# Optimization experiments

Measured on AMD Instinct MI355X. Metric: run time of the kernel, lower is better.

## Reference

```python
import jax, jax.numpy as jnp
import numpy as np

# Kernel codes matching style 'L;O2;P2;Y2,1,1;R0.5;W1,1'
KERNEL_CODES = ['L', 'O', 'P', 'Y', 'R', 'W']
SM_TEMP = 1.0


def _norm_sq(q, k):
    # q: [n,l,h,e], k: [n,s,h,e] -> [n,h,l,s]
    q2 = jnp.einsum('nlhe,nlhe->nhl', q, q)[..., None]        # [n,h,l,1]
    k2 = jnp.einsum('nshe,nshe->nhs', k, k)[:, :, None, :]     # [n,h,1,s]
    qk = jnp.einsum('nlhe,nshe->nhls', q, k)
    return q2 + k2 - 2.0 * qk


def _kernel(code, q, k):
    if code == 'L':
        return jnp.einsum('nlhe,nshe->nhls', q, k)
    if code == 'O':  # -log(1 + ns^(p/2)), p=2
        return -jnp.log1p(_norm_sq(q, k))
    if code == 'P':  # -(ns)^(p/2), p=2
        return -_norm_sq(q, k)
    if code == 'Y':  # (alpha*<q,k> + c)^p, p=2, alpha=1, c=1
        d = jnp.einsum('nlhe,nshe->nhls', q, k)
        return (d + 1.0) ** 2
    if code == 'R':  # exp(-gamma*ns), gamma=0.5
        return jnp.exp(-0.5 * _norm_sq(q, k))
    if code == 'W':  # cos(ns/a)*exp(-ns/b), a=b=1
        ns = _norm_sq(q, k)
        return jnp.cos(ns) * jnp.exp(-ns)
    raise ValueError(code)


def setup_inputs() -> dict:
    key = jax.random.key(0)
    k1, k2, k3, k4 = jax.random.split(key, 4)
    N, L, S, H, E, K = 2, 1024, 1024, 8, 64, 6
    return {
        'query': jax.random.normal(k1, (N, L, H, E), dtype=jnp.float32),
        'key': jax.random.normal(k2, (N, S, H, E), dtype=jnp.float32),
        'attn_mask_add': jnp.zeros((N, L, S), dtype=jnp.float32),
        'key_lengths_add': jnp.zeros((N, S), dtype=jnp.float32),
        'M': jax.random.uniform(k3, (H, E, K), dtype=jnp.float32),
        'C': jax.random.uniform(k4, (K, H, E, E), dtype=jnp.float32),
    }


def reference(query, key, attn_mask_add, key_lengths_add, M, C):
    # mixture weights pi: [n,l,h,k]
    pi = jax.nn.softmax(jnp.einsum('nlhe,hek->nlhk', query, M), axis=-1)
    out = None
    for c, code in enumerate(KERNEL_CODES):
        # htilde = tanh(query @ C[c]): [n,l,h,e]
        htilde = jnp.tanh(jnp.einsum('nlhe,hef->nlhf', query, C[c]))
        qk = _kernel(code, htilde, key)                    # [n,h,l,s]
        qk = qk + attn_mask_add[:, None] + key_lengths_add[:, None, None, :]
        sm = jax.nn.softmax(SM_TEMP * qk, axis=-1)
        w = jnp.transpose(pi[..., c], (0, 2, 1))[..., None]  # [n,h,l,1]
        term = sm * w
        out = term if out is None else out + term
    return out
```

## Files before the change

kernel.cpp:

```cpp
#include <hip/hip_runtime.h>
#include <hip/hip_bf16.h>
#include <math.h>

#define N_  2
#define H_  8
#define G_  16
#define L_  1024
#define S_  1024
#define E_  64
#define NC_ 6

typedef __attribute__((ext_vector_type(4))) float floatx4;
typedef __attribute__((ext_vector_type(8))) short short8;

#define MFMA16 __builtin_amdgcn_mfma_f32_16x16x32_bf16

#define AHAT_OFF   0
#define AHAT_BYTES (NC_*G_*L_*128*2)
#define KHAT_OFF   (AHAT_OFF + AHAT_BYTES)
#define KHAT_BYTES (G_*S_*128*2)
#define PI_OFF     (KHAT_OFF + KHAT_BYTES)
#define PI_BYTES   (NC_*G_*L_*4)
#define HSQ_OFF    (PI_OFF + PI_BYTES)
#define HSQ_BYTES  (NC_*G_*L_*4)
#define KSQ_OFF    (HSQ_OFF + HSQ_BYTES)
#define KSQ_BYTES  (G_*S_*4)

__device__ __forceinline__ float ftanh(float x) {
  return 1.0f - 2.0f * __builtin_amdgcn_rcpf(__expf(2.0f*x) + 1.0f);
}

__global__ __launch_bounds__(256, 2) void k_prep(
    const float* __restrict__ q, const float* __restrict__ C,
    const float* __restrict__ key, const float* __restrict__ M,
    __hip_bfloat16* __restrict__ Ahat, float* __restrict__ hsq,
    __hip_bfloat16* __restrict__ Khat, float* __restrict__ ksq,
    float* __restrict__ pi_t) {
  extern __shared__ char smraw[];
  const int bx = blockIdx.x;
  const int t = threadIdx.x;

  if (bx < 768) {
    float* qs = (float*)smraw;
    float* Cs = qs + 128*68;
    const int g = bx / 48, r6 = bx % 48, c = r6 >> 3, lch = r6 & 7;
    const int n = g >> 3, h = g & 7;
    const int l0 = lch * 128;

    for (int u = t; u < 2048; u += 256) {
      int row = u >> 4, seg = u & 15;
      *(float4*)(qs + row*68 + seg*4) =
        *(const float4*)(q + (((size_t)(n*L_ + l0 + row))*H_ + h)*E_ + seg*4);
    }
    for (int u = t; u < 1024; u += 256) {
      int e = u >> 4, seg = u & 15;
      *(float4*)(Cs + e*68 + seg*4) =
        *(const float4*)(C + (((size_t)(c*8 + h))*64 + e)*64 + seg*4);
    }
    __syncthreads();

    const int rg = t >> 3, fg = t & 7;
    float acc[4][8];
    #pragma unroll
    for (int i = 0; i < 4; i++)
      #pragma unroll
      for (int j = 0; j < 8; j++) acc[i][j] = 0.0f;

    #pragma unroll 2
    for (int e0 = 0; e0 < 64; e0 += 4) {
      float4 q4[4];
      #pragma unroll
      for (int i = 0; i < 4; i++)
        q4[i] = *(const float4*)(qs + (rg*4 + i)*68 + e0);
      #pragma unroll
      for (int ee = 0; ee < 4; ee++) {
        float4 ca = *(const float4*)(Cs + (e0+ee)*68 + fg*8);
        float4 cb = *(const float4*)(Cs + (e0+ee)*68 + fg*8 + 4);
        float c8[8] = {ca.x, ca.y, ca.z, ca.w, cb.x, cb.y, cb.z, cb.w};
        #pragma unroll
        for (int i = 0; i < 4; i++) {
          float qv = (ee == 0) ? q4[i].x : (ee == 1) ? q4[i].y
                   : (ee == 2) ? q4[i].z : q4[i].w;
          #pragma unroll
          for (int j = 0; j < 8; j++) acc[i][j] = fmaf(qv, c8[j], acc[i][j]);
        }
      }
    }

    #pragma unroll
    for (int i = 0; i < 4; i++) {
      int l = l0 + rg*4 + i;
      size_t rowb = (((size_t)(c*G_ + g))*L_ + l) * 128;
      float ss = 0.0f;
      short8 hi8, lo8;
      #pragma unroll
      for (int j = 0; j < 8; j++) {
        float hv = ftanh(acc[i][j]);
        ss += hv*hv;
        __hip_bfloat16 hi = __float2bfloat16(hv);
        __hip_bfloat16 lo = __float2bfloat16(hv - __bfloat162float(hi));
        short hs, ls;
        __builtin_memcpy(&hs, &hi, 2);
        __builtin_memcpy(&ls, &lo, 2);
        hi8[j] = hs; lo8[j] = ls;
      }
      *(short8*)((char*)Ahat + (rowb + fg*8)*2)      = hi8;
      *(short8*)((char*)Ahat + (rowb + 64 + fg*8)*2) = lo8;
      ss += __shfl_xor(ss, 1); ss += __shfl_xor(ss, 2); ss += __shfl_xor(ss, 4);
      if (fg == 0) hsq[((size_t)(c*G_ + g))*L_ + l] = ss;
    }
  } else if (bx < 1024) {
    const int kb = bx - 768;
    const int wv = t >> 6, lane = t & 63;
    #pragma unroll 2
    for (int it = 0; it < 16; it++) {
      int r = kb*64 + it*4 + wv;
      int g = r >> 10, s = r & 1023, n = g >> 3, h = g & 7;
      float v = key[(((size_t)(n*S_ + s))*H_ + h)*E_ + lane];
      __hip_bfloat16 hi = __float2bfloat16(v);
      __hip_bfloat16 lo = __float2bfloat16(v - __bfloat162float(hi));
      size_t base = ((size_t)g*S_ + s)*128;
      Khat[base + lane]      = hi;
      Khat[base + 64 + lane] = lo;
      float sq = v*v;
      #pragma unroll
      for (int off = 32; off; off >>= 1) sq += __shfl_xor(sq, off);
      if (lane == 0) ksq[(size_t)g*S_ + s] = sq;
    }
  } else {
    float* Ms = (float*)smraw;
    const int pb = bx - 1024;
    const int g = pb >> 2, lch = pb & 3;
    const int n = g >> 3, h = g & 7;
    const int l = lch*256 + t;
    for (int u = t; u < 384; u += 256) Ms[u] = M[h*384 + u];
    __syncthreads();
    const float* qrow = q + (((size_t)(n*L_ + l))*H_ + h)*E_;
    float p[6] = {0.f, 0.f, 0.f, 0.f, 0.f, 0.f};
    #pragma unroll 8
    for (int e = 0; e < 64; e++) {
      float qv = qrow[e];
      #pragma unroll
      for (int k = 0; k < 6; k++) p[k] = fmaf(qv, Ms[e*6 + k], p[k]);
    }
    float mx = p[0];
    #pragma unroll
    for (int k = 1; k < 6; k++) mx = fmaxf(mx, p[k]);
    float den = 0.f;
    #pragma unroll
    for (int k = 0; k < 6; k++) den += __expf(p[k] - mx);
    float rden = __builtin_amdgcn_rcpf(den);
    #pragma unroll
    for (int k = 0; k < 6; k++)
      pi_t[((size_t)(k*G_ + g))*L_ + l] = __expf(p[k] - mx) * rden;
  }
}

#define LDS_A6LO  0
#define LDS_ZRED  13824
#define LDS_MRED  15360
#define LDS_CST   16896
#define LDS_TOTAL 17664

__global__ __launch_bounds__(256, 2) void k_main(
    const __hip_bfloat16* __restrict__ Ahat, const __hip_bfloat16* __restrict__ Khat,
    const float* __restrict__ hsq, const float* __restrict__ ksq,
    const float* __restrict__ mask, const float* __restrict__ klen,
    const float* __restrict__ pi_t, float* __restrict__ out) {
  extern __shared__ char smraw[];
  char*   A6     = smraw + LDS_A6LO;
  float*  zred   = (float*)(smraw + LDS_ZRED);
  float*  mred   = (float*)(smraw + LDS_MRED);
  float2* cst    = (float2*)(smraw + LDS_CST);

  const int l0 = blockIdx.x * 16; const int g = blockIdx.y; const int n = g >> 3;
  const int t = threadIdx.x; const int w = t >> 6; const int lane = t & 63;
  const int quad = lane >> 4; const int lc = lane & 15;

  #pragma unroll
  for (int rep = 0; rep < 3; rep++) {
    int u = t + rep*256; int row = u >> 3, seg = u & 7;
    int cc = row >> 4, lr = row & 15;
    *(int4*)(A6 + row*144 + seg*16) =
      *(const int4*)((const char*)Ahat +
          (((size_t)(cc*G_ + g))*L_ + l0 + lr)*256 + 128 + seg*16);
  }

  short8 ah[6][2];
  #pragma unroll
  for (int cc = 0; cc < 6; cc++) {
    const char* arow = (const char*)Ahat + (((size_t)(cc*G_ + g))*L_ + l0 + lc)*256;
    ah[cc][0] = *(const short8*)(arow + quad*16);
    ah[cc][1] = *(const short8*)(arow + 64 + quad*16);
  }

  float h1p = 1.0f  + hsq[((size_t)(1*G_ + g))*L_ + l0 + lc];
  float nh2 = 64.0f - hsq[((size_t)(2*G_ + g))*L_ + l0 + lc];
  float h4h = -0.5f * hsq[((size_t)(4*G_ + g))*L_ + l0 + lc];
  float nh5 = -hsq[((size_t)(5*G_ + g))*L_ + l0 + lc];

  __syncthreads();

  auto LOADK = [&](int st, short8 (&bf)[4]) {
    const char* base = (const char*)Khat +
        (((size_t)g)*S_ + st*64 + w*16 + lc)*256 + quad*16;
    #pragma unroll
    for (int kt = 0; kt < 4; kt++)
      bf[kt] = *(const short8*)(base + kt*64);
  };

  float Zc0 = 0.f, Zc1 = 0.f, Zc2 = 0.f, Zc3 = 0.f, zp = 0.f;
  float m3 = -INFINITY, z3 = 0.f;

  auto SWEEP1 = [&](int st, const short8 (&bf)[4]) {
    int sb = st*64 + w*16 + quad*4;
    float4 mk4 = *(const float4*)(mask + ((size_t)(n*L_ + l0 + lc))*S_ + sb);
    float4 kl4 = *(const float4*)(klen + (size_t)n*S_ + sb);
    float4 kq4 = *(const float4*)(ksq  + (size_t)g*S_ + sb);
    float kq[4] = {kq4.x, kq4.y, kq4.z, kq4.w};
    float mv[4], Ev[4];
    mv[0] = mk4.x + kl4.x; mv[1] = mk4.y + kl4.y;
    mv[2] = mk4.z + kl4.z; mv[3] = mk4.w + kl4.w;
    #pragma unroll
    for (int i = 0; i < 4; i++) Ev[i] = __expf(mv[i]);
    #pragma unroll
    for (int c = 0; c < 6; c++) {
      short8 al0 = *(const short8*)(A6 + (c*16 + lc)*144 + quad*16);
      short8 al1 = *(const short8*)(A6 + (c*16 + lc)*144 + 64 + quad*16);
      floatx4 a = {0.f, 0.f, 0.f, 0.f};
      a = MFMA16(bf[0], ah[c][0], a, 0,0,0);
      a = MFMA16(bf[1], ah[c][1], a, 0,0,0);
      a = MFMA16(bf[0], al0,      a, 0,0,0);
      a = MFMA16(bf[1], al1,      a, 0,0,0);
      a = MFMA16(bf[2], ah[c][0], a, 0,0,0);
      a = MFMA16(bf[3], ah[c][1], a, 0,0,0);
      #pragma unroll
      for (int i = 0; i < 4; i++) {
        float d = a[i];
        if (c == 0) {
          Zc0 = fmaf(Ev[i], __expf(d), Zc0);
        } else if (c == 1) {
          Zc1 = fmaf(Ev[i], __builtin_amdgcn_rcpf(fmaf(-2.f, d, h1p + kq[i])), Zc1);
        } else if (c == 2) {
          zp += __expf(fmaf(2.f, d, nh2 - kq[i] + mv[i]));
        } else if (c == 3) {
          float tt = d + 1.f;
          float x  = fmaf(tt, tt, mv[i]);
          float mn = fmaxf(m3, x);
          float e  = __expf(fminf(m3, x) - mn);
          z3 = (x > m3) ? fmaf(z3, e, 1.0f) : (z3 + e);
          m3 = mn;
        } else if (c == 4) {
          Zc2 = fmaf(Ev[i], __expf(__expf(d + fmaf(-0.5f, kq[i], h4h))), Zc2);
        } else {
          float a5 = fmaf(2.f, d, nh5 - kq[i]);
          Zc3 = fmaf(Ev[i], __expf(__cosf(a5) * __expf(a5)), Zc3);
        }
      }
    }
  };

  {
    short8 bA[4], bB[4];
    LOADK(0, bA);
    #pragma unroll 1
    for (int st = 0; st < 16; st += 2) {
      LOADK(st + 1, bB);
      SWEEP1(st, bA);
      LOADK((st + 2) & 15, bA);
      SWEEP1(st + 1, bB);
    }
  }

  #pragma unroll
  for (int off = 16; off < 64; off <<= 1) {
    Zc0 += __shfl_xor(Zc0, off); Zc1 += __shfl_xor(Zc1, off);
    Zc2 += __shfl_xor(Zc2, off); Zc3 += __shfl_xor(Zc3, off);
    zp  += __shfl_xor(zp,  off);
    float mo = __shfl_xor(m3, off);
    float zo = __shfl_xor(z3, off);
    float mn = fmaxf(m3, mo);
    float e  = __expf(fminf(m3, mo) - mn);
    z3 = (mo > m3) ? fmaf(z3, e, zo) : fmaf(zo, e, z3);
    m3 = mn;
  }
  if (lane < 16) {
    zred[w*96 + 0*16 + lc] = Zc0; mred[w*96 + 0*16 + lc] = 0.f;
    zred[w*96 + 1*16 + lc] = Zc1; mred[w*96 + 1*16 + lc] = 0.f;
    zred[w*96 + 2*16 + lc] = zp;  mred[w*96 + 2*16 + lc] = 0.f;
    zred[w*96 + 3*16 + lc] = z3;  mred[w*96 + 3*16 + lc] = m3;
    zred[w*96 + 4*16 + lc] = Zc2; mred[w*96 + 4*16 + lc] = 0.f;
    zred[w*96 + 5*16 + lc] = Zc3; mred[w*96 + 5*16 + lc] = 0.f;
  }
  __syncthreads();
  if (t < 96) {
    int c = t >> 4;
    float z = zred[t], m = mred[t];
    if (c == 3) {
      #pragma unroll
      for (int w2 = 1; w2 < 4; w2++) {
        float mo = mred[w2*96 + t], zo = zred[w2*96 + t];
        float mn = fmaxf(m, mo);
        float e  = __expf(fminf(m, mo) - mn);
        z = (mo > m) ? fmaf(z, e, zo) : fmaf(zo, e, z);
        m = mn;
      }
    } else {
      #pragma unroll
      for (int w2 = 1; w2 < 4; w2++) z += zred[w2*96 + t];
    }
    float piv = pi_t[((size_t)((t >> 4)*G_ + g))*L_ + l0 + (t & 15)];
    cst[t] = make_float2(piv / z, m);
  }
  __syncthreads();

  float ac0 = cst[0*16 + lc].x, ac1 = cst[1*16 + lc].x, ac2 = cst[2*16 + lc].x;
  float ac3 = cst[3*16 + lc].x, ac4 = cst[4*16 + lc].x, ac5 = cst[5*16 + lc].x;
  float m3f = cst[3*16 + lc].y;

  auto SWEEP2 = [&](int st, const short8 (&bf)[4]) {
    int sb = st*64 + w*16 + quad*4;
    float4 mk4 = *(const float4*)(mask + ((size_t)(n*L_ + l0 + lc))*S_ + sb);
    float4 kl4 = *(const float4*)(klen + (size_t)n*S_ + sb);
    float4 kq4 = *(const float4*)(ksq  + (size_t)g*S_ + sb);
    float kq[4] = {kq4.x, kq4.y, kq4.z, kq4.w};
    float mv[4], Ev[4];
    mv[0] = mk4.x + kl4.x; mv[1] = mk4.y + kl4.y;
    mv[2] = mk4.z + kl4.z; mv[3] = mk4.w + kl4.w;
    #pragma unroll
    for (int i = 0; i < 4; i++) Ev[i] = __expf(mv[i]);
    float Sacc[4] = {0.f, 0.f, 0.f, 0.f};
    float Gg[4]   = {0.f, 0.f, 0.f, 0.f};
    #pragma unroll
    for (int c = 0; c < 6; c++) {
      short8 al0 = *(const short8*)(A6 + (c*16 + lc)*144 + quad*16);
      short8 al1 = *(const short8*)(A6 + (c*16 + lc)*144 + 64 + quad*16);
      floatx4 a = {0.f, 0.f, 0.f, 0.f};
      a = MFMA16(bf[0], ah[c][0], a, 0,0,0);
      a = MFMA16(bf[1], ah[c][1], a, 0,0,0);
      a = MFMA16(bf[0], al0,      a, 0,0,0);
      a = MFMA16(bf[1], al1,      a, 0,0,0);
      a = MFMA16(bf[2], ah[c][0], a, 0,0,0);
      a = MFMA16(bf[3], ah[c][1], a, 0,0,0);
      #pragma unroll
      for (int i = 0; i < 4; i++) {
        float d = a[i];
        if (c == 0) {
          Sacc[i] = fmaf(ac0, __expf(d), Sacc[i]);
        } else if (c == 1) {
          Sacc[i] = fmaf(ac1, __builtin_amdgcn_rcpf(fmaf(-2.f, d, h1p + kq[i])), Sacc[i]);
        } else if (c == 2) {
          Gg[i] = fmaf(ac2, __expf(fmaf(2.f, d, nh2 - kq[i] + mv[i])), Gg[i]);
        } else if (c == 3) {
          float tt = d + 1.f;
          float x  = fmaf(tt, tt, mv[i]);
          Gg[i] = fmaf(ac3, __expf(x - m3f), Gg[i]);
        } else if (c == 4) {
          Sacc[i] = fmaf(ac4, __expf(__expf(d + fmaf(-0.5f, kq[i], h4h))), Sacc[i]);
        } else {
          float a5 = fmaf(2.f, d, nh5 - kq[i]);
          Sacc[i] = fmaf(ac5, __expf(__cosf(a5) * __expf(a5)), Sacc[i]);
        }
      }
    }
    float4 ov;
    ov.x = fmaf(Ev[0], Sacc[0], Gg[0]);
    ov.y = fmaf(Ev[1], Sacc[1], Gg[1]);
    ov.z = fmaf(Ev[2], Sacc[2], Gg[2]);
    ov.w = fmaf(Ev[3], Sacc[3], Gg[3]);
    *(float4*)(out + (((size_t)g)*L_ + l0 + lc)*S_ + sb) = ov;
  };

  {
    short8 bA[4], bB[4];
    LOADK(0, bA);
    #pragma unroll 1
    for (int st = 0; st < 16; st += 2) {
      LOADK(st + 1, bB);
      SWEEP2(st, bA);
      LOADK((st + 2) & 15, bA);
      SWEEP2(st + 1, bB);
    }
  }
}

extern "C" void kernel_launch(void* const* d_in, const int* in_sizes, int n_in,
                              void* d_out, int out_size, void* d_ws, size_t ws_size,
                              hipStream_t stream) {
  (void)in_sizes; (void)n_in; (void)out_size; (void)ws_size;
  const float* q    = (const float*)d_in[0];
  const float* key  = (const float*)d_in[1];
  const float* mask = (const float*)d_in[2];
  const float* klen = (const float*)d_in[3];
  const float* M    = (const float*)d_in[4];
  const float* C    = (const float*)d_in[5];
  char* ws = (char*)d_ws;
  __hip_bfloat16* Ahat = (__hip_bfloat16*)(ws + AHAT_OFF);
  __hip_bfloat16* Khat = (__hip_bfloat16*)(ws + KHAT_OFF);
  float* pi_t    = (float*)(ws + PI_OFF);
  float* hsq     = (float*)(ws + HSQ_OFF);
  float* ksq     = (float*)(ws + KSQ_OFF);
  float* out = (float*)d_out;

  k_prep<<<1088, 256, 52224, stream>>>(q, C, key, M, Ahat, hsq, Khat, ksq, pi_t);
  k_main<<<dim3(64, 16), 256, LDS_TOTAL, stream>>>(Ahat, Khat, hsq, ksq, mask, klen,
                                                   pi_t, out);
}
```

Baseline: 199.6 us.

## Compute htilde projection in prep kernel with split-bf16 MFMA instead of FP32 FMA

Replaces the LDS-tiled FP32 FMA matmul for query@C[c] with 16x16x32 bf16 MFMAs, using a hi/lo split (three products) to keep near-FP32 accuracy. Each wave now processes 16 rows across three of the six mixture components, reusing the query fragments it holds in registers. Dynamic shared memory for the prep kernel goes away and the grid shrinks from 1088 to 832 blocks. In exchange, C is loaded with strided, uncoalesced scalar reads and converted again for every tile, and Ahat is written with scalar 2-byte stores instead of vector stores.

Measured after the change: 207.2 us. 3.8% more time.

```diff
diff --git a/kernel.cpp b/kernel.cpp
--- a/kernel.cpp
+++ b/kernel.cpp
@@ -30,112 +30,111 @@
   return 1.0f - 2.0f * __builtin_amdgcn_rcpf(__expf(2.0f*x) + 1.0f);
 }
 
-__global__ __launch_bounds__(256, 2) void k_prep(
+__global__ __launch_bounds__(256) void k_prep(
     const float* __restrict__ q, const float* __restrict__ C,
     const float* __restrict__ key, const float* __restrict__ M,
     __hip_bfloat16* __restrict__ Ahat, float* __restrict__ hsq,
     __hip_bfloat16* __restrict__ Khat, float* __restrict__ ksq,
     float* __restrict__ pi_t) {
-  extern __shared__ char smraw[];
+  __shared__ float Ms[384];
   const int bx = blockIdx.x;
   const int t = threadIdx.x;
-
-  if (bx < 768) {
-    float* qs = (float*)smraw;
-    float* Cs = qs + 128*68;
-    const int g = bx / 48, r6 = bx % 48, c = r6 >> 3, lch = r6 & 7;
+  const int w = t >> 6, lane = t & 63;
+  const int quad = lane >> 4, lc = lane & 15;
+
+  if (bx < 512) {
+    const int g = bx >> 5, lch = bx & 31;
     const int n = g >> 3, h = g & 7;
-    const int l0 = lch * 128;
-
-    for (int u = t; u < 2048; u += 256) {
-      int row = u >> 4, seg = u & 15;
-      *(float4*)(qs + row*68 + seg*4) =
-        *(const float4*)(q + (((size_t)(n*L_ + l0 + row))*H_ + h)*E_ + seg*4);
-    }
-    for (int u = t; u < 1024; u += 256) {
-      int e = u >> 4, seg = u & 15;
-      *(float4*)(Cs + e*68 + seg*4) =
-        *(const float4*)(C + (((size_t)(c*8 + h))*64 + e)*64 + seg*4);
-    }
-    __syncthreads();
-
-    const int rg = t >> 3, fg = t & 7;
-    float acc[4][8];
-    #pragma unroll
-    for (int i = 0; i < 4; i++)
-      #pragma unroll
-      for (int j = 0; j < 8; j++) acc[i][j] = 0.0f;
-
-    #pragma unroll 2
-    for (int e0 = 0; e0 < 64; e0 += 4) {
-      float4 q4[4];
-      #pragma unroll
-      for (int i = 0; i < 4; i++)
-        q4[i] = *(const float4*)(qs + (rg*4 + i)*68 + e0);
-      #pragma unroll
-      for (int ee = 0; ee < 4; ee++) {
-        float4 ca = *(const float4*)(Cs + (e0+ee)*68 + fg*8);
-        float4 cb = *(const float4*)(Cs + (e0+ee)*68 + fg*8 + 4);
-        float c8[8] = {ca.x, ca.y, ca.z, ca.w, cb.x, cb.y, cb.z, cb.w};
+    const int lt = lch*32 + (w >> 1)*16;
+    const int c0 = (w & 1)*3;
+
+    short8 qh[2], ql[2];
+    #pragma unroll
+    for (int kc = 0; kc < 2; kc++) {
+      const float* qp = q + (((size_t)(n*L_ + lt + lc))*H_ + h)*E_ + kc*32 + quad*8;
+      float4 a0 = *(const float4*)qp, a1 = *(const float4*)(qp + 4);
+      float v[8] = {a0.x,a0.y,a0.z,a0.w,a1.x,a1.y,a1.z,a1.w};
+      #pragma unroll
+      for (int j = 0; j < 8; j++) {
+        __hip_bfloat16 hb = __float2bfloat16(v[j]);
+        __hip_bfloat16 lb = __float2bfloat16(v[j] - __bfloat162float(hb));
+        short hs, ls;
+        __builtin_memcpy(&hs, &hb, 2); __builtin_memcpy(&ls, &lb, 2);
+        qh[kc][j] = hs; ql[kc][j] = ls;
+      }
+    }
+
+    #pragma unroll 1
+    for (int cc = 0; cc < 3; cc++) {
+      const int c = c0 + cc;
+      const float* Cb = C + ((size_t)(c*8 + h))*64*64;
+      float ss[4] = {0.f, 0.f, 0.f, 0.f};
+      #pragma unroll 2
+      for (int ft = 0; ft < 4; ft++) {
+        short8 bh[2], bl[2];
+        #pragma unroll
+        for (int kc = 0; kc < 2; kc++)
+          #pragma unroll
+          for (int j = 0; j < 8; j++) {
+            float cv = Cb[(size_t)(kc*32 + quad*8 + j)*64 + ft*16 + lc];
+            __hip_bfloat16 hb = __float2bfloat16(cv);
+            __hip_bfloat16 lb = __float2bfloat16(cv - __bfloat162float(hb));
+            short hs, ls;
+            __builtin_memcpy(&hs, &hb, 2); __builtin_memcpy(&ls, &lb, 2);
+            bh[kc][j] = hs; bl[kc][j] = ls;
+          }
+        floatx4 d = {0.f, 0.f, 0.f, 0.f};
+        d = MFMA16(qh[0], bh[0], d, 0,0,0);
+        d = MFMA16(qh[1], bh[1], d, 0,0,0);
+        d = MFMA16(qh[0], bl[0], d, 0,0,0);
+        d = MFMA16(qh[1], bl[1], d, 0,0,0);
+        d = MFMA16(ql[0], bh[0], d, 0,0,0);
+        d = MFMA16(ql[1], bh[1], d, 0,0,0);
         #pragma unroll
         for (int i = 0; i < 4; i++) {
-          float qv = (ee == 0) ? q4[i].x : (ee == 1) ? q4[i].y
-                   : (ee == 2) ? q4[i].z : q4[i].w;
-          #pragma unroll
-          for (int j = 0; j < 8; j++) acc[i][j] = fmaf(qv, c8[j], acc[i][j]);
+          float hv = ftanh(d[i]);
+          ss[i] += hv*hv;
+          __hip_bfloat16 hb = __float2bfloat16(hv);
+          __hip_bfloat16 lb = __float2bfloat16(hv - __bfloat162float(hb));
+          char* rowp = (char*)Ahat +
+              (((size_t)(c*G_ + g))*L_ + lt + quad*4 + i)*256;
+          *(__hip_bfloat16*)(rowp + (ft*16 + lc)*2)       = hb;
+          *(__hip_bfloat16*)(rowp + 128 + (ft*16 + lc)*2) = lb;
         }
       }
-    }
-
-    #pragma unroll
-    for (int i = 0; i < 4; i++) {
-      int l = l0 + rg*4 + i;
-      size_t rowb = (((size_t)(c*G_ + g))*L_ + l) * 128;
-      float ss = 0.0f;
-      short8 hi8, lo8;
-      #pragma unroll
-      for (int j = 0; j < 8; j++) {
-        float hv = ftanh(acc[i][j]);
-        ss += hv*hv;
-        __hip_bfloat16 hi = __float2bfloat16(hv);
-        __hip_bfloat16 lo = __float2bfloat16(hv - __bfloat162float(hi));
-        short hs, ls;
-        __builtin_memcpy(&hs, &hi, 2);
-        __builtin_memcpy(&ls, &lo, 2);
-        hi8[j] = hs; lo8[j] = ls;
-      }
-      *(short8*)((char*)Ahat + (rowb + fg*8)*2)      = hi8;
-      *(short8*)((char*)Ahat + (rowb + 64 + fg*8)*2) = lo8;
-      ss += __shfl_xor(ss, 1); ss += __shfl_xor(ss, 2); ss += __shfl_xor(ss, 4);
-      if (fg == 0) hsq[((size_t)(c*G_ + g))*L_ + l] = ss;
-    }
-  } else if (bx < 1024) {
-    const int kb = bx - 768;
-    const int wv = t >> 6, lane = t & 63;
+      #pragma unroll
+      for (int i = 0; i < 4; i++) {
+        float s = ss[i];
+        s += __shfl_xor(s, 1); s += __shfl_xor(s, 2);
+        s += __shfl_xor(s, 4); s += __shfl_xor(s, 8);
+        if (lc == 0) hsq[((size_t)(c*G_ + g))*L_ + lt + quad*4 + i] = s;
+      }
+    }
+  } else if (bx < 768) {
+    const int kb = bx - 512;
     #pragma unroll 2
     for (int it = 0; it < 16; it++) {
-      int r = kb*64 + it*4 + wv;
-      int g = r >> 10, s = r & 1023, n = g >> 3, h = g & 7;
-      float v = key[(((size_t)(n*S_ + s))*H_ + h)*E_ + lane];
+      int r = kb*64 + it*4 + w;
+      int kg = r >> 10, s = r & 1023, kn = kg >> 3, kh = kg & 7;
+      float v = key[(((size_t)(kn*S_ + s))*H_ + kh)*E_ + lane];
       __hip_bfloat16 hi = __float2bfloat16(v);
       __hip_bfloat16 lo = __float2bfloat16(v - __bfloat162float(hi));
-      size_t base = ((size_t)g*S_ + s)*128;
+      size_t base = ((size_t)kg*S_ + s)*128;
       Khat[base + lane]      = hi;
       Khat[base + 64 + lane] = lo;
       float sq = v*v;
       #pragma unroll
       for (int off = 32; off; off >>= 1) sq += __shfl_xor(sq, off);
-      if (lane == 0) ksq[(size_t)g*S_ + s] = sq;
+      if (lane == 0) ksq[(size_t)kg*S_ + s] = sq;
     }
   } else {
-    float* Ms = (float*)smraw;
-    const int pb = bx - 1024;
-    const int g = pb >> 2, lch = pb & 3;
-    const int n = g >> 3, h = g & 7;
+    const int pb = bx - 768;
+    const int pg = pb >> 2, lch = pb & 3;
+    const int pn = pg >> 3, ph = pg & 7;
     const int l = lch*256 + t;
-    for (int u = t; u < 384; u += 256) Ms[u] = M[h*384 + u];
+    for (int u = t; u < 384; u += 256) Ms[u] = M[ph*384 + u];
     __syncthreads();
-    const float* qrow = q + (((size_t)(n*L_ + l))*H_ + h)*E_;
+    const float* qrow = q + (((size_t)(pn*L_ + l))*H_ + ph)*E_;
     float p[6] = {0.f, 0.f, 0.f, 0.f, 0.f, 0.f};
     #pragma unroll 8
     for (int e = 0; e < 64; e++) {
@@ -152,7 +151,7 @@
     float rden = __builtin_amdgcn_rcpf(den);
     #pragma unroll
     for (int k = 0; k < 6; k++)
-      pi_t[((size_t)(k*G_ + g))*L_ + l] = __expf(p[k] - mx) * rden;
+      pi_t[((size_t)(k*G_ + pg))*L_ + l] = __expf(p[k] - mx) * rden;
   }
 }
 
@@ -402,7 +401,7 @@
   float* ksq     = (float*)(ws + KSQ_OFF);
   float* out = (float*)d_out;
 
-  k_prep<<<1088, 256, 52224, stream>>>(q, C, key, M, Ahat, hsq, Khat, ksq, pi_t);
+  k_prep<<<832, 256, 0, stream>>>(q, C, key, M, Ahat, hsq, Khat, ksq, pi_t);
   k_main<<<dim3(64, 16), 256, LDS_TOTAL, stream>>>(Ahat, Khat, hsq, ksq, mask, klen,
                                                    pi_t, out);
 }
```
